# Optimization experiments

Hardware: AMD Instinct MI355X
Metric: run time of the kernel (lower is better)

Reference implementation:

```python
import jax, jax.numpy as jnp
import numpy as np


def setup_inputs() -> dict:
    key = jax.random.key(0)
    ks = jax.random.split(key, 4)
    B, C, H, W = 4, 512, 64, 64
    A = 512  # attention_dim
    x = jax.random.normal(ks[0], (B, C, H, W), dtype=jnp.float32)
    # 1x1 conv weights as [out_ch, in_ch] matrices (kaiming-like scale)
    scale = np.sqrt(2.0 / C).astype(np.float32)
    Wq = jax.random.normal(ks[1], (A, C), dtype=jnp.float32) * scale
    Wk = jax.random.normal(ks[2], (A, C), dtype=jnp.float32) * scale
    Wv = jax.random.normal(ks[3], (C, C), dtype=jnp.float32) * scale
    bq = jnp.zeros((A,), dtype=jnp.float32)
    bk = jnp.zeros((A,), dtype=jnp.float32)
    bv = jnp.zeros((C,), dtype=jnp.float32)
    return {"x": x, "Wq": Wq, "bq": bq, "Wk": Wk, "bk": bk, "Wv": Wv, "bv": bv}


def reference(x, Wq, bq, Wk, bk, Wv, bv):
    B, C, H, W = x.shape
    N = H * W
    xf = x.reshape(B, C, N)  # [B, C, N]
    # 1x1 convs == per-pixel channel matmuls
    q = jnp.einsum('ac,bcn->bna', Wq, xf) + bq[None, None, :]   # [B, N, A] (query, permuted)
    k = jnp.einsum('ac,bcn->ban', Wk, xf) + bk[None, :, None]   # [B, A, N] (key)
    v = jnp.einsum('oc,bcn->bno', Wv, xf) + bv[None, None, :]   # [B, N, C] (value, permuted)
    attn = jnp.einsum('bna,bam->bnm', q, k)                     # [B, N, N]
    attn = jax.nn.softmax(attn, axis=-2)                        # softmax over dim=-2 (queries)
    out = jnp.einsum('bnm,bmc->bnc', attn, v)                   # [B, N, C]
    # Faithful to torch: .view(B, C, H, W) reinterprets the [B, N, C] buffer
    out = out.reshape(B, C, H, W)
    return x + 0.1 * out
```

## Files before the change

### kernel.cpp

```cpp
#include <hip/hip_runtime.h>
#include <stdint.h>


#define LDT 40
#define SUB 5120

typedef _Float16 f16x8 __attribute__((ext_vector_type(8)));
typedef float f32x4 __attribute__((ext_vector_type(4)));

__device__ __forceinline__ void async16(const _Float16* g, _Float16* l)
{
  __builtin_amdgcn_global_load_lds(
      (const __attribute__((address_space(1))) void*)g,
      (__attribute__((address_space(3))) void*)l, 16, 0, 0);
}

#define WVM(N) asm volatile("s_waitcnt vmcnt(" #N ")" ::: "memory")

template <int ASRC, int EPI, int NSUB, int STG, int OCC>
__global__ void __launch_bounds__(256, OCC) gemm_f16(
    const _Float16* __restrict__ Ap, long lda, long zsa,
    const _Float16* __restrict__ Bp, long ldb, long zsb,
    int kslice,
    const _Float16* __restrict__ fs16, long zsl,
    float* __restrict__ outF, _Float16* __restrict__ outH, long ldc, long zso,
    const float* __restrict__ bias0, const float* __restrict__ bias1,
    const float* __restrict__ xadd,
    float* __restrict__ pmax, float* __restrict__ psum, long zsp,
    float alpha)
{
  constexpr int SMEM_E = (STG == 1) ? (NSUB * 8192 + (ASRC == 1 ? 4096 : 0))
                                    : (2 * NSUB * SUB);
  __shared__ _Float16 smem[SMEM_E];

  const int z = blockIdx.z;
  const long i0 = (long)blockIdx.x * 128;
  const long j0 = (long)blockIdx.y * 128;
  const int t = (int)threadIdx.x;
  const int lane = t & 63;
  const int wv = t >> 6;
  const int quad = lane >> 4;
  const int lrow = lane & 15;
  const int wm = (wv & 1) << 6;
  const int wn = (wv >> 1) << 6;

  f32x4 acc[4][4];
  const f32x4 fz = {0.f, 0.f, 0.f, 0.f};
#pragma unroll
  for (int a = 0; a < 4; a++)
#pragma unroll
    for (int b = 0; b < 4; b++) acc[a][b] = fz;

  if constexpr (STG == 0) {
    const int r0 = t >> 2;
    const int s0 = (t & 3) << 3;

    const _Float16* gA0 = Ap + z * zsa + (i0 + r0) * lda + s0;
    const _Float16* gA1 = gA0 + 64 * lda;
    const _Float16* gB0 = Bp + z * zsb + (j0 + r0) * ldb + s0;
    const _Float16* gB1 = gB0 + 64 * ldb;
    const int la0 = r0 * LDT + s0;
    const int la1 = (r0 + 64) * LDT + s0;

    for (int kk = 0; kk < kslice; kk += 32 * NSUB) {
      f16x8 va[NSUB][2], vb[NSUB][2];
#pragma unroll
      for (int s = 0; s < NSUB; s++) {
        va[s][0] = *(const f16x8*)(gA0 + kk + 32 * s);
        va[s][1] = *(const f16x8*)(gA1 + kk + 32 * s);
        vb[s][0] = *(const f16x8*)(gB0 + kk + 32 * s);
        vb[s][1] = *(const f16x8*)(gB1 + kk + 32 * s);
      }
      __syncthreads();
#pragma unroll
      for (int s = 0; s < NSUB; s++) {
        *(f16x8*)&smem[s * SUB + la0] = va[s][0];
        *(f16x8*)&smem[s * SUB + la1] = va[s][1];
        *(f16x8*)&smem[(NSUB + s) * SUB + la0] = vb[s][0];
        *(f16x8*)&smem[(NSUB + s) * SUB + la1] = vb[s][1];
      }
      __syncthreads();

#pragma unroll
      for (int h = 0; h < NSUB; h++) {
        const _Float16* pA = smem + h * SUB;
        const _Float16* pB = smem + (NSUB + h) * SUB;
        f16x8 fa[4], fb[4];
#pragma unroll
        for (int f = 0; f < 4; f++) {
          fa[f] = *(const f16x8*)&pA[(wm + f * 16 + lrow) * LDT + quad * 8];
          fb[f] = *(const f16x8*)&pB[(wn + f * 16 + lrow) * LDT + quad * 8];
        }
#pragma unroll
        for (int fm = 0; fm < 4; fm++)
#pragma unroll
          for (int fn = 0; fn < 4; fn++)
            acc[fm][fn] = __builtin_amdgcn_mfma_f32_16x16x32_f16(fa[fm], fb[fn], acc[fm][fn], 0, 0, 0);
      }
    }
  } else {
    const int crow = lane >> 2;
    const int ks8 = (((lane & 3) ^ ((lane >> 3) & 3)) << 3);

    const _Float16* gAc0 = Ap + z * zsa + (i0 + 16 * wv + crow) * lda + ks8;
    const _Float16* gAc1 = gAc0 + 64 * lda;
    const _Float16* gBc0 = Bp + z * zsb + (j0 + 16 * wv + crow) * ldb + ks8;
    const _Float16* gBc1 = gBc0 + 64 * ldb;

    const int qs = ((quad ^ ((lrow >> 1) & 3)) << 3);

    auto stage = [&](int buf, int kk2) {
      _Float16* base = smem + buf * 8192;
      async16(gAc0 + kk2, base + wv * 512);
      async16(gAc1 + kk2, base + 2048 + wv * 512);
      async16(gBc0 + kk2, base + 4096 + wv * 512);
      async16(gBc1 + kk2, base + 6144 + wv * 512);
    };

    _Float16* fsL = nullptr;
    if constexpr (ASRC == 1) {
      fsL = smem + NSUB * 8192;
      const _Float16* fsrc = fs16 + z * zsl + (long)blockIdx.x * 4096;
      *(f16x8*)&fsL[t * 16] = *(const f16x8*)&fsrc[t * 16];
      *(f16x8*)&fsL[t * 16 + 8] = *(const f16x8*)&fsrc[t * 16 + 8];
    }
    stage(0, 0);
    if constexpr (NSUB == 4) { stage(1, 32); stage(2, 64); }
    if constexpr (ASRC == 1)
      asm volatile("s_waitcnt lgkmcnt(0)" ::: "memory");
    __builtin_amdgcn_s_barrier();

    int ib = 0;
    for (int kk = 0; kk < kslice; kk += 32, ++ib) {
      const int rem = kslice - kk;
      if constexpr (NSUB == 4) {
        if (rem > 96) { stage((ib + 3) & 3, kk + 96); WVM(12); }
        else if (rem > 64) { WVM(8); }
        else if (rem > 32) { WVM(4); }
        else { WVM(0); }
      } else {
        if (rem > 32) { stage((ib + 1) & 1, kk + 32); WVM(4); }
        else { WVM(0); }
      }
      __builtin_amdgcn_s_barrier();

      const int cur = ib & (NSUB - 1);
      const _Float16* pA = smem + cur * 8192;
      const _Float16* pB = pA + 4096;
      f16x8 fa[4], fb[4];
#pragma unroll
      for (int f = 0; f < 4; f++) {
        fa[f] = *(const f16x8*)&pA[(wm + f * 16 + lrow) * 32 + qs];
        fb[f] = *(const f16x8*)&pB[(wn + f * 16 + lrow) * 32 + qs];
      }
      if constexpr (ASRC == 1) {
        const f16x8 fsv = *(const f16x8*)&fsL[kk + quad * 8];
#pragma unroll
        for (int f = 0; f < 4; f++) fa[f] = fa[f] * fsv;
      }
#pragma unroll
      for (int fm = 0; fm < 4; fm++)
#pragma unroll
        for (int fn = 0; fn < 4; fn++)
          acc[fm][fn] = __builtin_amdgcn_mfma_f32_16x16x32_f16(fa[fm], fb[fn], acc[fm][fn], 0, 0, 0);

      __builtin_amdgcn_s_barrier();
    }
  }

  const long obase = (long)z * zso;

  if constexpr (EPI == 1 || EPI == 2) {
#pragma unroll
    for (int fm = 0; fm < 4; fm++) {
      const long gi0 = i0 + wm + fm * 16 + quad * 4;
#pragma unroll
      for (int fn = 0; fn < 4; fn++) {
        const long gj = j0 + wn + fn * 16 + lrow;
        float badd = 0.f;
        if constexpr (EPI == 1) badd = (gj < 512) ? bias0[gj] : bias1[gj - 512];
#pragma unroll
        for (int r = 0; r < 4; r++) {
          float v = acc[fm][fn][r];
          if constexpr (EPI == 1) v += badd;
          else v += bias0[gi0 + r];
          outH[obase + (gi0 + r) * ldc + gj] = (_Float16)v;
        }
      }
    }
  } else if constexpr (EPI == 3) {
#pragma unroll
    for (int fm = 0; fm < 4; fm++) {
      const long gi0 = i0 + wm + fm * 16 + quad * 4;
#pragma unroll
      for (int fn = 0; fn < 4; fn++) {
        const long gj = j0 + wn + fn * 16 + lrow;
#pragma unroll
        for (int r = 0; r < 4; r++) {
          const long o = obase + (gi0 + r) * ldc + gj;
          outF[o] = fmaf(alpha, acc[fm][fn][r], xadd[o]);
        }
      }
    }
  } else {
    __syncthreads();
    float* Ls = (float*)smem;
#pragma unroll
    for (int fn = 0; fn < 4; fn++) {
      float mx = -3.4e38f;
#pragma unroll
      for (int fm = 0; fm < 4; fm++)
#pragma unroll
        for (int r = 0; r < 4; r++) mx = fmaxf(mx, acc[fm][fn][r]);
      Ls[(wv * 4 + quad) * 64 + fn * 16 + lrow] = mx;
    }
    __syncthreads();
    {
      const int c = t & 127;
      const int h = t >> 7;
      const int wvv = ((c >> 6) << 1) + h;
      const int wc = c & 63;
      float M = -3.4e38f;
#pragma unroll
      for (int q = 0; q < 4; q++) M = fmaxf(M, Ls[(wvv * 4 + q) * 64 + wc]);
      Ls[1024 + h * 128 + c] = M;
    }
    __syncthreads();
    if (t < 128) {
      float Mcol = fmaxf(Ls[1024 + t], Ls[1152 + t]);
      pmax[z * zsp + (long)blockIdx.x * 4096 + j0 + t] = Mcol;
      Ls[1280 + t] = Mcol;
    }
    __syncthreads();
#pragma unroll
    for (int fn = 0; fn < 4; fn++) {
      const int colc = wn + fn * 16 + lrow;
      const float Mcol = Ls[1280 + colc];
      const long gj = j0 + colc;
      float sm = 0.f;
#pragma unroll
      for (int fm = 0; fm < 4; fm++) {
        const long gi0 = i0 + wm + fm * 16 + quad * 4;
#pragma unroll
        for (int r = 0; r < 4; r++) {
          float e = __expf(acc[fm][fn][r] - Mcol);
          sm += e;
          outH[obase + (gi0 + r) * ldc + gj] = (_Float16)e;
        }
      }
      Ls[(wv * 4 + quad) * 64 + fn * 16 + lrow] = sm;
    }
    __syncthreads();
    if (t < 128) {
      const int wc = t & 63;
      const int ch = t >> 6;
      float s = 0.f;
#pragma unroll
      for (int h = 0; h < 2; h++) {
        const int wvv = (ch << 1) + h;
#pragma unroll
        for (int q = 0; q < 4; q++) s += Ls[(wvv * 4 + q) * 64 + wc];
      }
      psum[z * zsp + (long)blockIdx.x * 4096 + j0 + t] = s;
    }
  }
}

__global__ void convert_weights(const float* __restrict__ Wq, const float* __restrict__ Wk,
                                const float* __restrict__ Wv,
                                _Float16* __restrict__ WQK, _Float16* __restrict__ Wv16)
{
  int idx = blockIdx.x * 256 + threadIdx.x;
  if (idx < 524288)
    WQK[idx] = (_Float16)((idx < 262144) ? Wq[idx] : Wk[idx - 262144]);
  else
    Wv16[idx - 524288] = (_Float16)Wv[idx - 524288];
}

__global__ void transpose_x(const float* __restrict__ x, _Float16* __restrict__ xT)
{
  __shared__ float tile[32][33];
  const int b = blockIdx.z;
  const int n0 = blockIdx.x * 32;
  const int c0 = blockIdx.y * 32;
  const int tx = threadIdx.x;
  const int ty = threadIdx.y;
  const float* xb = x + (long)b * 2097152;
#pragma unroll
  for (int k = 0; k < 4; k++)
    tile[ty + k * 8][tx] = xb[(long)(c0 + ty + k * 8) * 4096 + n0 + tx];
  __syncthreads();
  _Float16* xTb = xT + (long)b * 2097152;
#pragma unroll
  for (int k = 0; k < 4; k++)
    xTb[(long)(n0 + ty + k * 8) * 512 + c0 + tx] = (_Float16)tile[tx][ty + k * 8];
}

__global__ void stats_scale(const float* __restrict__ pmax, const float* __restrict__ psum,
                            _Float16* __restrict__ fs16)
{
  const int idx = blockIdx.x * 256 + threadIdx.x;
  const int z = idx >> 12;
  const int m = idx & 4095;
  const float* pm = pmax + (long)z * 131072 + m;
  const float* ps = psum + (long)z * 131072 + m;
  float M = -3.4e38f, S = 0.f;
  for (int i = 0; i < 32; i++) {
    float m2 = pm[(long)i * 4096], s2 = ps[(long)i * 4096];
    float nm = fmaxf(M, m2);
    S = S * __expf(M - nm) + s2 * __expf(m2 - nm);
    M = nm;
  }
  const float lse = M + __logf(S);
  _Float16* fo = fs16 + (long)z * 131072 + m;
  for (int i = 0; i < 32; i++)
    fo[(long)i * 4096] = (_Float16)__expf(pm[(long)i * 4096] - lse);
}

extern "C" void kernel_launch(void* const* d_in, const int* in_sizes, int n_in,
                              void* d_out, int out_size, void* d_ws, size_t ws_size,
                              hipStream_t stream)
{
  const float* x  = (const float*)d_in[0];
  const float* Wq = (const float*)d_in[1];
  const float* bq = (const float*)d_in[2];
  const float* Wk = (const float*)d_in[3];
  const float* bk = (const float*)d_in[4];
  const float* Wv = (const float*)d_in[5];
  const float* bv = (const float*)d_in[6];
  float* out = (float*)d_out;

  char* w = (char*)d_ws;
  _Float16* WQK   = (_Float16*)(w + 0);
  _Float16* Wv16  = (_Float16*)(w + 1048576);
  _Float16* xT    = (_Float16*)(w + 1572864);
  _Float16* QK    = (_Float16*)(w + 18350080);
  _Float16* Vt    = (_Float16*)(w + 51904512);
  float*    pmaxB = (float*)   (w + 68747264);
  float*    psumB = (float*)   (w + 70844416);
  _Float16* fs16  = (_Float16*)(w + 72941568);
  _Float16* S16   = (_Float16*)(w + 75038720);

  convert_weights<<<3072, 256, 0, stream>>>(Wq, Wk, Wv, WQK, Wv16);
  transpose_x<<<dim3(128, 16, 4), dim3(32, 8), 0, stream>>>(x, xT);

  gemm_f16<0, 1, 2, 0, 2><<<dim3(32, 8, 4), 256, 0, stream>>>(
      xT, 512, 2097152L, WQK, 512, 0L, 512, nullptr, 0L,
      nullptr, QK, 1024, 4194304L, bq, bk, nullptr, nullptr, nullptr, 0L, 0.f);
  gemm_f16<0, 2, 2, 0, 2><<<dim3(4, 32, 4), 256, 0, stream>>>(
      Wv16, 512, 0L, xT, 512, 2097152L, 512, nullptr, 0L,
      nullptr, Vt, 4096, 2097152L, bv, nullptr, nullptr, nullptr, nullptr, 0L, 0.f);
  gemm_f16<0, 4, 2, 1, 4><<<dim3(32, 32, 4), 256, 0, stream>>>(
      QK, 1024, 4194304L, QK + 512, 1024, 4194304L, 512, nullptr, 0L,
      nullptr, S16, 4096, 16777216L, nullptr, nullptr, nullptr,
      pmaxB, psumB, 131072L, 0.f);
  stats_scale<<<64, 256, 0, stream>>>(pmaxB, psumB, fs16);
  gemm_f16<1, 3, 4, 1, 2><<<dim3(32, 4, 4), 256, 0, stream>>>(
      S16, 4096, 16777216L, Vt, 4096, 2097152L, 4096, fs16, 131072L,
      out, nullptr, 512, 2097152L, nullptr, nullptr, x, nullptr, nullptr, 0L, 0.1f);
}
```

Before: 319.9 us.

## Add double-buffered multi-subtile async LDS pipeline and retune GEMM configs

Adds a new STG==2 GEMM mainloop that stages NSUB 32-wide K subtiles per step into a double-buffered LDS region using async global-to-LDS loads. The next step's loads are issued before the current step's compute, with a single barrier pair per step. The final attention-times-V GEMM moves to this path with NSUB=2, and the scale factors are loaded per step. The Q/K and V projection GEMMs switch from the register-staged path to the async STG==1 path with a higher occupancy bound. The cost is more LDS per block and different occupancy behaviour.

```diff
diff --git a/kernel.cpp b/kernel.cpp
--- a/kernel.cpp
+++ b/kernel.cpp
@@ -30,6 +30,7 @@
     float alpha)
 {
   constexpr int SMEM_E = (STG == 1) ? (NSUB * 8192 + (ASRC == 1 ? 4096 : 0))
+                       : (STG == 2) ? (4 * NSUB * 4096)
                                     : (2 * NSUB * SUB);
   __shared__ _Float16 smem[SMEM_E];
 
@@ -98,7 +99,7 @@
             acc[fm][fn] = __builtin_amdgcn_mfma_f32_16x16x32_f16(fa[fm], fb[fn], acc[fm][fn], 0, 0, 0);
       }
     }
-  } else {
+  } else if constexpr (STG == 1) {
     const int crow = lane >> 2;
     const int ks8 = (((lane & 3) ^ ((lane >> 3) & 3)) << 3);
 
@@ -165,6 +166,77 @@
           acc[fm][fn] = __builtin_amdgcn_mfma_f32_16x16x32_f16(fa[fm], fb[fn], acc[fm][fn], 0, 0, 0);
 
       __builtin_amdgcn_s_barrier();
+    }
+  } else {
+    constexpr int KSTEP = 32 * NSUB;
+    constexpr int BUFE = 2 * NSUB * 4096;
+    const int crow = lane >> 2;
+    const int ks8 = (((lane & 3) ^ ((lane >> 3) & 3)) << 3);
+
+    const _Float16* gAc0 = Ap + z * zsa + (i0 + 16 * wv + crow) * lda + ks8;
+    const _Float16* gAc1 = gAc0 + 64 * lda;
+    const _Float16* gBc0 = Bp + z * zsb + (j0 + 16 * wv + crow) * ldb + ks8;
+    const _Float16* gBc1 = gBc0 + 64 * ldb;
+    _Float16* ldsC0 = smem + wv * 512;
+    _Float16* ldsC1 = smem + (wv + 4) * 512;
+
+    const _Float16* fsZq = nullptr;
+    if constexpr (ASRC == 1)
+      fsZq = fs16 + z * zsl + (long)blockIdx.x * 4096 + quad * 8;
+
+    const int qs = ((quad ^ ((lrow >> 1) & 3)) << 3);
+
+    auto stage = [&](int buf, int kk) {
+#pragma unroll
+      for (int s = 0; s < NSUB; s++) {
+        const int ab = buf * BUFE + s * 4096;
+        const int bb = buf * BUFE + (NSUB + s) * 4096;
+        async16(gAc0 + kk + 32 * s, ldsC0 + ab);
+        async16(gAc1 + kk + 32 * s, ldsC1 + ab);
+        async16(gBc0 + kk + 32 * s, ldsC0 + bb);
+        async16(gBc1 + kk + 32 * s, ldsC1 + bb);
+      }
+    };
+
+    stage(0, 0);
+    int cur = 0;
+    for (int kk = 0; kk < kslice; kk += KSTEP) {
+      f16x8 fsv[NSUB];
+      if constexpr (ASRC == 1) {
+#pragma unroll
+        for (int h = 0; h < NSUB; h++)
+          fsv[h] = *(const f16x8*)(fsZq + kk + 32 * h);
+      }
+      if (kk + KSTEP < kslice) {
+        stage(cur ^ 1, kk + KSTEP);
+        WVM(8);
+      } else {
+        WVM(0);
+      }
+      __builtin_amdgcn_s_barrier();
+
+#pragma unroll
+      for (int h = 0; h < NSUB; h++) {
+        const _Float16* pA = smem + cur * BUFE + h * 4096;
+        const _Float16* pB = smem + cur * BUFE + (NSUB + h) * 4096;
+        f16x8 fa[4], fb[4];
+#pragma unroll
+        for (int f = 0; f < 4; f++) {
+          fa[f] = *(const f16x8*)&pA[(wm + f * 16 + lrow) * 32 + qs];
+          fb[f] = *(const f16x8*)&pB[(wn + f * 16 + lrow) * 32 + qs];
+        }
+        if constexpr (ASRC == 1) {
+#pragma unroll
+          for (int f = 0; f < 4; f++) fa[f] = fa[f] * fsv[h];
+        }
+#pragma unroll
+        for (int fm = 0; fm < 4; fm++)
+#pragma unroll
+          for (int fn = 0; fn < 4; fn++)
+            acc[fm][fn] = __builtin_amdgcn_mfma_f32_16x16x32_f16(fa[fm], fb[fn], acc[fm][fn], 0, 0, 0);
+      }
+      __builtin_amdgcn_s_barrier();
+      cur ^= 1;
     }
   }
 
@@ -344,10 +416,10 @@
   convert_weights<<<3072, 256, 0, stream>>>(Wq, Wk, Wv, WQK, Wv16);
   transpose_x<<<dim3(128, 16, 4), dim3(32, 8), 0, stream>>>(x, xT);
 
-  gemm_f16<0, 1, 2, 0, 2><<<dim3(32, 8, 4), 256, 0, stream>>>(
+  gemm_f16<0, 1, 2, 1, 4><<<dim3(32, 8, 4), 256, 0, stream>>>(
       xT, 512, 2097152L, WQK, 512, 0L, 512, nullptr, 0L,
       nullptr, QK, 1024, 4194304L, bq, bk, nullptr, nullptr, nullptr, 0L, 0.f);
-  gemm_f16<0, 2, 2, 0, 2><<<dim3(4, 32, 4), 256, 0, stream>>>(
+  gemm_f16<0, 2, 2, 1, 4><<<dim3(4, 32, 4), 256, 0, stream>>>(
       Wv16, 512, 0L, xT, 512, 2097152L, 512, nullptr, 0L,
       nullptr, Vt, 4096, 2097152L, bv, nullptr, nullptr, nullptr, nullptr, 0L, 0.f);
   gemm_f16<0, 4, 2, 1, 4><<<dim3(32, 32, 4), 256, 0, stream>>>(
@@ -355,7 +427,7 @@
       nullptr, S16, 4096, 16777216L, nullptr, nullptr, nullptr,
       pmaxB, psumB, 131072L, 0.f);
   stats_scale<<<64, 256, 0, stream>>>(pmaxB, psumB, fs16);
-  gemm_f16<1, 3, 4, 1, 2><<<dim3(32, 4, 4), 256, 0, stream>>>(
+  gemm_f16<1, 3, 2, 2, 2><<<dim3(32, 4, 4), 256, 0, stream>>>(
       S16, 4096, 16777216L, Vt, 4096, 2097152L, 4096, fs16, 131072L,
       out, nullptr, 512, 2097152L, nullptr, nullptr, x, nullptr, nullptr, 0L, 0.1f);
 }
```

After: 318.7 us. No clear change (-0.4%).

## Load GEMM operands directly from global, stage only A via LDS

Applied to the files above, without the earlier changes.

The QK^T score GEMM now uses a new path (STG=3) that loads MFMA fragments straight from global memory with no LDS staging or barriers. The final attention-times-V GEMM (STG=4) stages only the S tile through a 4-deep async LDS ring with 64-wide k-steps. The V operand and the per-column softmax scale are read directly from global into registers, which removes the LDS copy of the scale and one barrier per iteration. The aim is to cut LDS traffic and synchronisation, at the cost of uncoalesced, cache-dependent global loads and more register pressure.

```diff
diff --git a/kernel.cpp b/kernel.cpp
--- a/kernel.cpp
+++ b/kernel.cpp
@@ -29,7 +29,8 @@
     float* __restrict__ pmax, float* __restrict__ psum, long zsp,
     float alpha)
 {
-  constexpr int SMEM_E = (STG == 1) ? (NSUB * 8192 + (ASRC == 1 ? 4096 : 0))
+  constexpr int SMEM_E = (STG == 3) ? 4096
+                       : (STG == 4) ? 32768
                                     : (2 * NSUB * SUB);
   __shared__ _Float16 smem[SMEM_E];
 
@@ -98,14 +99,40 @@
             acc[fm][fn] = __builtin_amdgcn_mfma_f32_16x16x32_f16(fa[fm], fb[fn], acc[fm][fn], 0, 0, 0);
       }
     }
+  } else if constexpr (STG == 3) {
+    const _Float16* gA[4];
+    const _Float16* gB[4];
+#pragma unroll
+    for (int f = 0; f < 4; f++) {
+      gA[f] = Ap + z * zsa + (i0 + wm + f * 16 + lrow) * lda + quad * 8;
+      gB[f] = Bp + z * zsb + (j0 + wn + f * 16 + lrow) * ldb + quad * 8;
+    }
+    for (int kk = 0; kk < kslice; kk += 32) {
+      f16x8 fa[4], fb[4];
+#pragma unroll
+      for (int f = 0; f < 4; f++) {
+        fa[f] = *(const f16x8*)(gA[f] + kk);
+        fb[f] = *(const f16x8*)(gB[f] + kk);
+      }
+#pragma unroll
+      for (int fm = 0; fm < 4; fm++)
+#pragma unroll
+        for (int fn = 0; fn < 4; fn++)
+          acc[fm][fn] = __builtin_amdgcn_mfma_f32_16x16x32_f16(fa[fm], fb[fn], acc[fm][fn], 0, 0, 0);
+    }
   } else {
     const int crow = lane >> 2;
     const int ks8 = (((lane & 3) ^ ((lane >> 3) & 3)) << 3);
 
     const _Float16* gAc0 = Ap + z * zsa + (i0 + 16 * wv + crow) * lda + ks8;
     const _Float16* gAc1 = gAc0 + 64 * lda;
-    const _Float16* gBc0 = Bp + z * zsb + (j0 + 16 * wv + crow) * ldb + ks8;
-    const _Float16* gBc1 = gBc0 + 64 * ldb;
+
+    const _Float16* gB[4];
+#pragma unroll
+    for (int f = 0; f < 4; f++)
+      gB[f] = Bp + z * zsb + (j0 + wn + f * 16 + lrow) * ldb + quad * 8;
+
+    const _Float16* fsZq = fs16 + z * zsl + (long)blockIdx.x * 4096 + quad * 8;
 
     const int qs = ((quad ^ ((lrow >> 1) & 3)) << 3);
 
@@ -113,58 +140,49 @@
       _Float16* base = smem + buf * 8192;
       async16(gAc0 + kk2, base + wv * 512);
       async16(gAc1 + kk2, base + 2048 + wv * 512);
-      async16(gBc0 + kk2, base + 4096 + wv * 512);
-      async16(gBc1 + kk2, base + 6144 + wv * 512);
+      async16(gAc0 + kk2 + 32, base + 4096 + wv * 512);
+      async16(gAc1 + kk2 + 32, base + 4096 + 2048 + wv * 512);
     };
 
-    _Float16* fsL = nullptr;
-    if constexpr (ASRC == 1) {
-      fsL = smem + NSUB * 8192;
-      const _Float16* fsrc = fs16 + z * zsl + (long)blockIdx.x * 4096;
-      *(f16x8*)&fsL[t * 16] = *(const f16x8*)&fsrc[t * 16];
-      *(f16x8*)&fsL[t * 16 + 8] = *(const f16x8*)&fsrc[t * 16 + 8];
-    }
     stage(0, 0);
-    if constexpr (NSUB == 4) { stage(1, 32); stage(2, 64); }
-    if constexpr (ASRC == 1)
-      asm volatile("s_waitcnt lgkmcnt(0)" ::: "memory");
-    __builtin_amdgcn_s_barrier();
+    stage(1, 64);
+    stage(2, 128);
 
     int ib = 0;
-    for (int kk = 0; kk < kslice; kk += 32, ++ib) {
+    for (int kk = 0; kk < kslice; kk += 64, ++ib) {
       const int rem = kslice - kk;
-      if constexpr (NSUB == 4) {
-        if (rem > 96) { stage((ib + 3) & 3, kk + 96); WVM(12); }
-        else if (rem > 64) { WVM(8); }
-        else if (rem > 32) { WVM(4); }
-        else { WVM(0); }
-      } else {
-        if (rem > 32) { stage((ib + 1) & 1, kk + 32); WVM(4); }
-        else { WVM(0); }
-      }
+      if (rem > 128) { WVM(8); }
+      else if (rem > 64) { WVM(4); }
+      else { WVM(0); }
       __builtin_amdgcn_s_barrier();
 
-      const int cur = ib & (NSUB - 1);
-      const _Float16* pA = smem + cur * 8192;
-      const _Float16* pB = pA + 4096;
-      f16x8 fa[4], fb[4];
-#pragma unroll
-      for (int f = 0; f < 4; f++) {
-        fa[f] = *(const f16x8*)&pA[(wm + f * 16 + lrow) * 32 + qs];
-        fb[f] = *(const f16x8*)&pB[(wn + f * 16 + lrow) * 32 + qs];
-      }
-      if constexpr (ASRC == 1) {
-        const f16x8 fsv = *(const f16x8*)&fsL[kk + quad * 8];
-#pragma unroll
-        for (int f = 0; f < 4; f++) fa[f] = fa[f] * fsv;
-      }
-#pragma unroll
-      for (int fm = 0; fm < 4; fm++)
-#pragma unroll
-        for (int fn = 0; fn < 4; fn++)
-          acc[fm][fn] = __builtin_amdgcn_mfma_f32_16x16x32_f16(fa[fm], fb[fn], acc[fm][fn], 0, 0, 0);
-
-      __builtin_amdgcn_s_barrier();
+      f16x8 fsv[2], fb[2][4];
+#pragma unroll
+      for (int h = 0; h < 2; h++) {
+        fsv[h] = *(const f16x8*)(fsZq + kk + 32 * h);
+#pragma unroll
+        for (int f = 0; f < 4; f++)
+          fb[h][f] = *(const f16x8*)(gB[f] + kk + 32 * h);
+      }
+      __builtin_amdgcn_sched_barrier(0);
+      if (rem > 192) stage((ib + 3) & 3, kk + 192);
+
+      const _Float16* pBuf = smem + (ib & 3) * 8192;
+#pragma unroll
+      for (int h = 0; h < 2; h++) {
+        const _Float16* pA = pBuf + h * 4096;
+        f16x8 fa[4];
+#pragma unroll
+        for (int f = 0; f < 4; f++) {
+          fa[f] = *(const f16x8*)&pA[(wm + f * 16 + lrow) * 32 + qs];
+          fa[f] = fa[f] * fsv[h];
+        }
+#pragma unroll
+        for (int fm = 0; fm < 4; fm++)
+#pragma unroll
+          for (int fn = 0; fn < 4; fn++)
+            acc[fm][fn] = __builtin_amdgcn_mfma_f32_16x16x32_f16(fa[fm], fb[h][fn], acc[fm][fn], 0, 0, 0);
+      }
     }
   }
 
@@ -350,12 +368,12 @@
   gemm_f16<0, 2, 2, 0, 2><<<dim3(4, 32, 4), 256, 0, stream>>>(
       Wv16, 512, 0L, xT, 512, 2097152L, 512, nullptr, 0L,
       nullptr, Vt, 4096, 2097152L, bv, nullptr, nullptr, nullptr, nullptr, 0L, 0.f);
-  gemm_f16<0, 4, 2, 1, 4><<<dim3(32, 32, 4), 256, 0, stream>>>(
+  gemm_f16<0, 4, 2, 3, 4><<<dim3(32, 32, 4), 256, 0, stream>>>(
       QK, 1024, 4194304L, QK + 512, 1024, 4194304L, 512, nullptr, 0L,
       nullptr, S16, 4096, 16777216L, nullptr, nullptr, nullptr,
       pmaxB, psumB, 131072L, 0.f);
   stats_scale<<<64, 256, 0, stream>>>(pmaxB, psumB, fs16);
-  gemm_f16<1, 3, 4, 1, 2><<<dim3(32, 4, 4), 256, 0, stream>>>(
+  gemm_f16<1, 3, 2, 4, 2><<<dim3(32, 4, 4), 256, 0, stream>>>(
       S16, 4096, 16777216L, Vt, 4096, 2097152L, 4096, fs16, 131072L,
       out, nullptr, 512, 2097152L, nullptr, nullptr, x, nullptr, nullptr, 0L, 0.1f);
 }
```

After: 532.7 us. 1.67x slower.
